# Kernel optimization log

Measured on AMD Instinct MI355X. Metric: run time of the kernel, lower is better.

The kernel has to match this reference:

```python
import jax, jax.numpy as jnp
import numpy as np

BETA = 0.25  # commitment-loss weight from init_kwargs

B, T, D, K = 16, 2048, 256, 1024


def setup_inputs() -> dict:
    key = jax.random.key(0)
    k1, k2 = jax.random.split(key)
    z_e = jax.random.normal(k1, (B, T, D), dtype=jnp.float32)
    codebook = jax.random.normal(k2, (K, D), dtype=jnp.float32)
    return {"z_e": z_e, "codebook": codebook}


def reference(z_e, codebook):
    # dot_z_embedding: tensordot over channel dim -> (B, T, K)
    dot = jnp.einsum("btd,kd->btk", z_e, codebook)
    norm_sq_z = jnp.sum(jnp.square(z_e), axis=-1, keepdims=True)      # (B, T, 1)
    norm_sq_e = jnp.sum(jnp.square(codebook), axis=-1)                # (K,)
    dist = -2.0 * dot + norm_sq_z + norm_sq_e                         # (B, T, K)
    ids = jnp.argmin(dist, axis=-1)                                   # (B, T) int
    z_q = codebook[ids]                                               # (B, T, D)
    # losses: tf.norm over the quantised axis, then mean
    loss_commit = jnp.mean(jnp.linalg.norm(jax.lax.stop_gradient(z_e) - z_q, axis=-1))
    loss_codebook = jnp.mean(jnp.linalg.norm(z_e - jax.lax.stop_gradient(z_q), axis=-1))
    loss_vq = loss_codebook + BETA * loss_commit
    similarity = dot / jnp.sqrt(norm_sq_z) / jnp.sqrt(norm_sq_e)      # (B, T, K) cosine
    return z_q, similarity, ids, loss_vq
```

## Files before the change

### kernel.cpp

```cpp
#include <hip/hip_runtime.h>


#define M_ROWS 32768
#define KCODES 1024
#define DDIM   256

typedef __bf16 bf16_t;
typedef __attribute__((ext_vector_type(8))) bf16_t bf16x8;
typedef __attribute__((ext_vector_type(4))) float f32x4;

__device__ __forceinline__ unsigned short f2bf(float f) {
  unsigned u = __float_as_uint(f);
  u += 0x7FFFu + ((u >> 16) & 1u);
  return (unsigned short)(u >> 16);
}

__device__ __forceinline__ float wave_sum(float p) {
#pragma unroll
  for (int o = 1; o < 64; o <<= 1) p += __shfl_xor(p, o);
  return p;
}
__device__ __forceinline__ float wave_min(float p) {
#pragma unroll
  for (int o = 1; o < 64; o <<= 1) p = fminf(p, __shfl_xor(p, o));
  return p;
}

__global__ __launch_bounds__(256) void prep_kernel(
    const float* __restrict__ ze, const float* __restrict__ cb,
    unsigned short* __restrict__ zb, unsigned short* __restrict__ cbb,
    float* __restrict__ sqz, float* __restrict__ rsqz,
    float* __restrict__ nse, float* __restrict__ sqe, float* __restrict__ rsqe)
{
  const int t = threadIdx.x;
  const int lane = t & 63;
  const int row = blockIdx.x * 4 + (t >> 6);
  if (row < M_ROWS) {
    const float4 z = ((const float4*)ze)[(size_t)row * 64 + lane];
    ushort4 u;
    u.x = f2bf(z.x); u.y = f2bf(z.y); u.z = f2bf(z.z); u.w = f2bf(z.w);
    ((ushort4*)zb)[(size_t)row * 64 + lane] = u;
    float p = wave_sum(z.x*z.x + z.y*z.y + z.z*z.z + z.w*z.w);
    if (lane == 0) { float s = sqrtf(p); sqz[row] = s; rsqz[row] = 1.0f / s; }
  } else {
    const int r = row - M_ROWS;
    const float4 e = ((const float4*)cb)[(size_t)r * 64 + lane];
    ushort4 u;
    u.x = f2bf(e.x); u.y = f2bf(e.y); u.z = f2bf(e.z); u.w = f2bf(e.w);
    ((ushort4*)cbb)[(size_t)r * 64 + lane] = u;
    float p = wave_sum(e.x*e.x + e.y*e.y + e.z*e.z + e.w*e.w);
    if (lane == 0) { nse[r] = p; float s = sqrtf(p); sqe[r] = s; rsqe[r] = 1.0f / s; }
  }
}

__global__ __launch_bounds__(256, 2) void gemm_sim_kernel(
    const unsigned short* __restrict__ zb, const unsigned short* __restrict__ cbb,
    const float* __restrict__ rsqz, const float* __restrict__ rsqe,
    float* __restrict__ sim)
{
  __shared__ __attribute__((aligned(128))) unsigned short lds[16384];
  const int tid  = threadIdx.x;
  const int wv   = tid >> 6, lane = tid & 63;
  const int bid  = blockIdx.x;
  const int swz  = (bid & 7) * 256 + (bid >> 3);
  const long row0 = (long)(swz >> 3) * 128;
  const int  col0 = (swz & 7) * 128;

  f32x4 acc[4][4] = {};

  const int rr = lane >> 3, qq = lane & 7;
  const int sq = ((qq ^ rr) << 3);

  for (int kt = 0; kt < 4; ++kt) {
    const int k0 = kt * 64;
#pragma unroll
    for (int i = 0; i < 4; ++i) {
      const int rbase = wv * 32 + i * 8;
      const unsigned short* srca = zb  + ((size_t)(row0 + rbase + rr)) * DDIM + k0 + sq;
      const unsigned short* srcb = cbb + ((size_t)(col0 + rbase + rr)) * DDIM + k0 + sq;
      __builtin_amdgcn_global_load_lds((const __attribute__((address_space(1))) void*)srca,
                                       (__attribute__((address_space(3))) void*)&lds[rbase * 64],
                                       16, 0, 0);
      __builtin_amdgcn_global_load_lds((const __attribute__((address_space(1))) void*)srcb,
                                       (__attribute__((address_space(3))) void*)&lds[8192 + rbase * 64],
                                       16, 0, 0);
    }
    __syncthreads();
    const int r16 = lane & 15, g = lane >> 4;
#pragma unroll
    for (int ks = 0; ks < 2; ++ks) {
      bf16x8 af[4], bfr[4];
#pragma unroll
      for (int mi = 0; mi < 4; ++mi) {
        const int r  = (wv >> 1) * 64 + mi * 16 + r16;
        const int qy = ((ks * 4 + g) ^ (r & 7)) << 4;
        af[mi] = *(const bf16x8*)((const char*)lds + r * 128 + qy);
      }
#pragma unroll
      for (int ni = 0; ni < 4; ++ni) {
        const int r  = (wv & 1) * 64 + ni * 16 + r16;
        const int qy = ((ks * 4 + g) ^ (r & 7)) << 4;
        bfr[ni] = *(const bf16x8*)((const char*)lds + 16384 + r * 128 + qy);
      }
#pragma unroll
      for (int mi = 0; mi < 4; ++mi)
#pragma unroll
        for (int ni = 0; ni < 4; ++ni)
          acc[mi][ni] = __builtin_amdgcn_mfma_f32_16x16x32_bf16(af[mi], bfr[ni], acc[mi][ni], 0, 0, 0);
    }
    __syncthreads();
  }

  const int r16 = lane & 15, g = lane >> 4;
  const int wm = wv >> 1, wn = wv & 1;
#pragma unroll
  for (int mi = 0; mi < 4; ++mi) {
#pragma unroll
    for (int j = 0; j < 4; ++j) {
      const long row = row0 + wm * 64 + mi * 16 + g * 4 + j;
      const float rz = rsqz[row];
      float* so = sim + (size_t)row * KCODES + col0 + wn * 64 + r16;
#pragma unroll
      for (int ni = 0; ni < 4; ++ni)
        so[ni * 16] = acc[mi][ni][j] * rz * rsqe[col0 + wn * 64 + ni * 16 + r16];
    }
  }
}

__global__ __launch_bounds__(256) void select_kernel(
    const float* __restrict__ ze, const float* __restrict__ cb,
    const float* __restrict__ sim, const float* __restrict__ sqz,
    const float* __restrict__ nse, const float* __restrict__ sqe,
    float* __restrict__ zq, float* __restrict__ ids, float* __restrict__ partials)
{
  __shared__ float s_nse[KCODES];
  __shared__ float s_sqe[KCODES];
  __shared__ float s_part[4];
  const int t = threadIdx.x;
  ((float4*)s_nse)[t] = ((const float4*)nse)[t];
  ((float4*)s_sqe)[t] = ((const float4*)sqe)[t];
  __syncthreads();

  const int lane = t & 63;
  const int row  = blockIdx.x * 4 + (t >> 6);
  const float4 zr = ((const float4*)ze)[(size_t)row * 64 + lane];
  const float  c2 = 2.0f * sqz[row];
  const float4* simr = (const float4*)(sim + (size_t)row * KCODES);

  float v[16];
  float vmin = INFINITY;
#pragma unroll
  for (int i = 0; i < 4; ++i) {
    const float4 s4 = simr[i * 64 + lane];
    const float sv[4] = {s4.x, s4.y, s4.z, s4.w};
#pragma unroll
    for (int c = 0; c < 4; ++c) {
      const int k = i * 256 + lane * 4 + c;
      const float val = s_nse[k] - c2 * s_sqe[k] * sv[c];
      v[i * 4 + c] = val;
      vmin = fminf(vmin, val);
    }
  }
  vmin = wave_min(vmin);
  const float lim = vmin + 1.0f;

  float tbest = INFINITY; int kbest = KCODES;
#pragma unroll
  for (int idx = 0; idx < 16; ++idx) {
    unsigned long long m = __ballot(v[idx] <= lim);
    const int i = idx >> 2, c = idx & 3;
    while (m) {
      const int lb = __ffsll(m) - 1;
      m &= m - 1;
      const int kc = i * 256 + lb * 4 + c;
      const float4 er = ((const float4*)cb)[(size_t)kc * 64 + lane];
      float p = wave_sum(zr.x*er.x + zr.y*er.y + zr.z*er.z + zr.w*er.w);
      const float tv = s_nse[kc] - 2.0f * p;
      if (tv < tbest || (tv == tbest && kc < kbest)) { tbest = tv; kbest = kc; }
    }
  }

  const float4 er = ((const float4*)cb)[(size_t)kbest * 64 + lane];
  ((float4*)zq)[(size_t)row * 64 + lane] = er;
  const float dx = zr.x - er.x, dy = zr.y - er.y, dz = zr.z - er.z, dw = zr.w - er.w;
  const float ss = wave_sum(dx*dx + dy*dy + dz*dz + dw*dw);
  if (lane == 0) {
    ids[row] = (float)kbest;
    s_part[t >> 6] = sqrtf(ss);
  }
  __syncthreads();
  if (t == 0)
    partials[blockIdx.x] = (s_part[0] + s_part[1]) + (s_part[2] + s_part[3]);
}

__global__ __launch_bounds__(256) void finalize_kernel(
    const float* __restrict__ partials, float* __restrict__ out_loss)
{
  __shared__ float s[4];
  const int t = threadIdx.x;
  float p = 0.0f;
#pragma unroll
  for (int i = 0; i < 32; ++i) p += partials[t + i * 256];
  p = wave_sum(p);
  if ((t & 63) == 0) s[t >> 6] = p;
  __syncthreads();
  if (t == 0) out_loss[0] = 1.25f * ((s[0] + s[1]) + (s[2] + s[3])) / 32768.0f;
}

extern "C" void kernel_launch(void* const* d_in, const int* in_sizes, int n_in,
                              void* d_out, int out_size, void* d_ws, size_t ws_size,
                              hipStream_t stream) {
  const float* ze = (const float*)d_in[0];
  const float* cb = (const float*)d_in[1];

  float* out  = (float*)d_out;
  float* zq   = out;
  float* sim  = out + 8388608;
  float* ids  = out + 41943040;
  float* lout = out + 41975808;

  char* w = (char*)d_ws;
  unsigned short* cbb = (unsigned short*)w;
  float* sqz  = (float*)(w + 524288);
  float* rsqz = (float*)(w + 655360);
  float* nse  = (float*)(w + 786432);
  float* sqe  = (float*)(w + 790528);
  float* rsqe = (float*)(w + 794624);
  float* partials = rsqz;

  unsigned short* zb = (unsigned short*)d_out;

  prep_kernel<<<8448, 256, 0, stream>>>(ze, cb, zb, cbb, sqz, rsqz, nse, sqe, rsqe);
  gemm_sim_kernel<<<2048, 256, 0, stream>>>(zb, cbb, rsqz, rsqe, sim);
  select_kernel<<<8192, 256, 0, stream>>>(ze, cb, sim, sqz, nse, sqe, zq, ids, partials);
  finalize_kernel<<<1, 256, 0, stream>>>(partials, lout);
}
```

Measured before the change: 78.30 us.

## Fuse per-tile top-2 candidate extraction into GEMM epilogue, skip similarity reread

The GEMM epilogue now computes quantized, index-encoded distances per row and keeps the top two candidates per 64-column tile, writing them to a small workspace buffer. A new select kernel reads these 32 candidates per row instead of the full 1024-wide similarity row and recomputes exact fp32 distances only for candidates within a margin. This removes the select kernel's read of the 128MB similarity matrix, at the cost of extra shuffle work in the GEMM epilogue. It falls back to the old path when the workspace is too small, and the top-2-per-tile pruning with a fixed margin could miss the true argmin in rare cases.

```diff
diff --git a/kernel.cpp b/kernel.cpp
--- a/kernel.cpp
+++ b/kernel.cpp
@@ -4,6 +4,7 @@
 #define M_ROWS 32768
 #define KCODES 1024
 #define DDIM   256
+#define ENC_BIG 33554432.0f
 
 typedef __bf16 bf16_t;
 typedef __attribute__((ext_vector_type(8))) bf16_t bf16x8;
@@ -56,7 +57,8 @@
 __global__ __launch_bounds__(256, 2) void gemm_sim_kernel(
     const unsigned short* __restrict__ zb, const unsigned short* __restrict__ cbb,
     const float* __restrict__ rsqz, const float* __restrict__ rsqe,
-    float* __restrict__ sim)
+    const float* __restrict__ nse,
+    float* __restrict__ sim, float* __restrict__ cand)
 {
   __shared__ __attribute__((aligned(128))) unsigned short lds[16384];
   const int tid  = threadIdx.x;
@@ -113,6 +115,7 @@
 
   const int r16 = lane & 15, g = lane >> 4;
   const int wm = wv >> 1, wn = wv & 1;
+
 #pragma unroll
   for (int mi = 0; mi < 4; ++mi) {
 #pragma unroll
@@ -125,9 +128,90 @@
         so[ni * 16] = acc[mi][ni][j] * rz * rsqe[col0 + wn * 64 + ni * 16 + r16];
     }
   }
-}
-
-__global__ __launch_bounds__(256) void select_kernel(
+
+  if (cand) {
+    float nsev[4];
+#pragma unroll
+    for (int ni = 0; ni < 4; ++ni) nsev[ni] = nse[col0 + wn * 64 + ni * 16 + r16];
+    const int tileIdx = ((col0 >> 6) | wn);
+#pragma unroll
+    for (int mi = 0; mi < 4; ++mi) {
+#pragma unroll
+      for (int j = 0; j < 4; ++j) {
+        float e1 = ENC_BIG, e2 = ENC_BIG;
+#pragma unroll
+        for (int ni = 0; ni < 4; ++ni) {
+          const float v = nsev[ni] - 2.0f * acc[mi][ni][j];
+          const float kf = (float)(col0 + wn * 64 + ni * 16 + r16);
+          const float enc = floorf((v + 1024.0f) * 8.0f) * 1024.0f + kf;
+          if (enc < e1) { e2 = e1; e1 = enc; } else e2 = fminf(e2, enc);
+        }
+#pragma unroll
+        for (int m = 1; m < 16; m <<= 1) {
+          const float p1 = __shfl_xor(e1, m);
+          const float p2 = __shfl_xor(e2, m);
+          const float n1 = fminf(e1, p1);
+          const float n2 = fminf(fmaxf(e1, p1), fminf(e2, p2));
+          e1 = n1; e2 = n2;
+        }
+        if (r16 == 0) {
+          const long row = row0 + wm * 64 + mi * 16 + g * 4 + j;
+          ((float2*)cand)[row * 16 + tileIdx] = make_float2(e1, e2);
+        }
+      }
+    }
+  }
+}
+
+__global__ __launch_bounds__(256) void select_fast_kernel(
+    const float* __restrict__ ze, const float* __restrict__ cb,
+    const float* __restrict__ cand, const float* __restrict__ nse,
+    float* __restrict__ zq, float* __restrict__ ids, float* __restrict__ partials)
+{
+  __shared__ float s_part[4];
+  const int t = threadIdx.x;
+  const int lane = t & 63;
+  const int row  = blockIdx.x * 4 + (t >> 6);
+
+  const float4 zr = ((const float4*)ze)[(size_t)row * 64 + lane];
+
+  const float* crow = cand + (size_t)row * 32;
+  float e = (lane < 32) ? crow[lane] : ENC_BIG;
+  const float m_enc = wave_min(e);
+  const float qmin  = floorf(m_enc * 0.0009765625f);
+  const float ql    = floorf(e * 0.0009765625f);
+
+  unsigned long long msk = __ballot(ql <= qmin + 16.0f);
+  int kbest;
+  if (__popcll(msk) == 1) {
+    kbest = ((int)m_enc) & 1023;
+  } else {
+    float tbest = INFINITY; kbest = KCODES;
+    while (msk) {
+      const int lb = __ffsll(msk) - 1;
+      msk &= msk - 1;
+      const int kc = ((int)__shfl(e, lb)) & 1023;
+      const float4 er = ((const float4*)cb)[(size_t)kc * 64 + lane];
+      const float p = wave_sum(zr.x*er.x + zr.y*er.y + zr.z*er.z + zr.w*er.w);
+      const float tv = nse[kc] - 2.0f * p;
+      if (tv < tbest || (tv == tbest && kc < kbest)) { tbest = tv; kbest = kc; }
+    }
+  }
+
+  const float4 er = ((const float4*)cb)[(size_t)kbest * 64 + lane];
+  ((float4*)zq)[(size_t)row * 64 + lane] = er;
+  const float dx = zr.x - er.x, dy = zr.y - er.y, dz = zr.z - er.z, dw = zr.w - er.w;
+  const float ss = wave_sum(dx*dx + dy*dy + dz*dz + dw*dw);
+  if (lane == 0) {
+    ids[row] = (float)kbest;
+    s_part[t >> 6] = sqrtf(ss);
+  }
+  __syncthreads();
+  if (t == 0)
+    partials[blockIdx.x] = (s_part[0] + s_part[1]) + (s_part[2] + s_part[3]);
+}
+
+__global__ __launch_bounds__(256) void select_full_kernel(
     const float* __restrict__ ze, const float* __restrict__ cb,
     const float* __restrict__ sim, const float* __restrict__ sqz,
     const float* __restrict__ nse, const float* __restrict__ sqe,
@@ -226,12 +310,19 @@
   float* nse  = (float*)(w + 786432);
   float* sqe  = (float*)(w + 790528);
   float* rsqe = (float*)(w + 794624);
+  float* cand = (float*)(w + 798720);
   float* partials = rsqz;
 
+  const bool fast = ws_size >= (size_t)(798720 + 4 * 1024 * 1024 + 256);
+
   unsigned short* zb = (unsigned short*)d_out;
 
   prep_kernel<<<8448, 256, 0, stream>>>(ze, cb, zb, cbb, sqz, rsqz, nse, sqe, rsqe);
-  gemm_sim_kernel<<<2048, 256, 0, stream>>>(zb, cbb, rsqz, rsqe, sim);
-  select_kernel<<<8192, 256, 0, stream>>>(ze, cb, sim, sqz, nse, sqe, zq, ids, partials);
+  gemm_sim_kernel<<<2048, 256, 0, stream>>>(zb, cbb, rsqz, rsqe, nse, sim,
+                                            fast ? cand : nullptr);
+  if (fast)
+    select_fast_kernel<<<8192, 256, 0, stream>>>(ze, cb, cand, nse, zq, ids, partials);
+  else
+    select_full_kernel<<<8192, 256, 0, stream>>>(ze, cb, sim, sqz, nse, sqe, zq, ids, partials);
   finalize_kernel<<<1, 256, 0, stream>>>(partials, lout);
 }
```

After: 72.85 us. -7.0%, faster.

## Fuse z prep, GEMM, argmin selection and loss into one kernel

Applied to the files above, without the earlier changes.

Merges the z-side prep, the similarity GEMM and the argmin/select pass into a single kernel. Each block now owns 64 rows across all 1024 codes, keeps the bf16 z tile resident in LDS, and computes top-2 quantised distance candidates per 64-column strip in the GEMM epilogue. This removes the bf16 z round-trip through global memory and the re-read of the 128 MB similarity matrix in the select pass. In exchange, the grid is only 512 blocks, the codebook is re-streamed per block with no double buffering, and a candidate may be missed when more than two near-ties fall in one strip.

```diff
diff --git a/kernel.cpp b/kernel.cpp
--- a/kernel.cpp
+++ b/kernel.cpp
@@ -4,6 +4,7 @@
 #define M_ROWS 32768
 #define KCODES 1024
 #define DDIM   256
+#define ENC_BIG 33554432.0f
 
 typedef __bf16 bf16_t;
 typedef __attribute__((ext_vector_type(8))) bf16_t bf16x8;
@@ -26,168 +27,181 @@
   return p;
 }
 
-__global__ __launch_bounds__(256) void prep_kernel(
-    const float* __restrict__ ze, const float* __restrict__ cb,
-    unsigned short* __restrict__ zb, unsigned short* __restrict__ cbb,
-    float* __restrict__ sqz, float* __restrict__ rsqz,
-    float* __restrict__ nse, float* __restrict__ sqe, float* __restrict__ rsqe)
+__global__ __launch_bounds__(256) void prep_cb_kernel(
+    const float* __restrict__ cb, unsigned short* __restrict__ cbb,
+    float* __restrict__ nse, float* __restrict__ rsqe)
 {
   const int t = threadIdx.x;
   const int lane = t & 63;
-  const int row = blockIdx.x * 4 + (t >> 6);
-  if (row < M_ROWS) {
-    const float4 z = ((const float4*)ze)[(size_t)row * 64 + lane];
+  const int r = blockIdx.x * 4 + (t >> 6);
+  const float4 e = ((const float4*)cb)[(size_t)r * 64 + lane];
+  ushort4 u;
+  u.x = f2bf(e.x); u.y = f2bf(e.y); u.z = f2bf(e.z); u.w = f2bf(e.w);
+  ((ushort4*)cbb)[(size_t)r * 64 + lane] = u;
+  float p = wave_sum(e.x*e.x + e.y*e.y + e.z*e.z + e.w*e.w);
+  if (lane == 0) { nse[r] = p; rsqe[r] = 1.0f / sqrtf(p); }
+}
+
+__global__ __launch_bounds__(256, 2) void fused_kernel(
+    const float* __restrict__ ze, const float* __restrict__ cb,
+    const unsigned short* __restrict__ cbb,
+    const float* __restrict__ nse_g, const float* __restrict__ rsqe_g,
+    float* __restrict__ sim, float* __restrict__ zq, float* __restrict__ ids,
+    float* __restrict__ partials)
+{
+  __shared__ __attribute__((aligned(128))) unsigned short A[64 * 256];
+  __shared__ __attribute__((aligned(128))) unsigned short Bt[128 * 64];
+  __shared__ float s_nse[KCODES];
+  __shared__ float s_rsqe[KCODES];
+  __shared__ float s_rsqz[64];
+  __shared__ float cand_lds[64 * 32];
+  __shared__ float s_part[4];
+
+  const int t = threadIdx.x;
+  const int wv = t >> 6, lane = t & 63;
+  const int r16 = lane & 15, g = lane >> 4;
+  const int wm = wv >> 1, wn = wv & 1;
+  const long row0 = (long)blockIdx.x * 64;
+
+  ((float4*)s_nse)[t]  = ((const float4*)nse_g)[t];
+  ((float4*)s_rsqe)[t] = ((const float4*)rsqe_g)[t];
+
+#pragma unroll
+  for (int k = 0; k < 16; ++k) {
+    const int row = wv + 4 * k;
+    const float4 z = ((const float4*)ze)[(row0 + row) * 64 + lane];
+    const float p = wave_sum(z.x*z.x + z.y*z.y + z.z*z.z + z.w*z.w);
+    if (lane == 0) s_rsqz[row] = 1.0f / sqrtf(p);
     ushort4 u;
     u.x = f2bf(z.x); u.y = f2bf(z.y); u.z = f2bf(z.z); u.w = f2bf(z.w);
-    ((ushort4*)zb)[(size_t)row * 64 + lane] = u;
-    float p = wave_sum(z.x*z.x + z.y*z.y + z.z*z.z + z.w*z.w);
-    if (lane == 0) { float s = sqrtf(p); sqz[row] = s; rsqz[row] = 1.0f / s; }
-  } else {
-    const int r = row - M_ROWS;
-    const float4 e = ((const float4*)cb)[(size_t)r * 64 + lane];
-    ushort4 u;
-    u.x = f2bf(e.x); u.y = f2bf(e.y); u.z = f2bf(e.z); u.w = f2bf(e.w);
-    ((ushort4*)cbb)[(size_t)r * 64 + lane] = u;
-    float p = wave_sum(e.x*e.x + e.y*e.y + e.z*e.z + e.w*e.w);
-    if (lane == 0) { nse[r] = p; float s = sqrtf(p); sqe[r] = s; rsqe[r] = 1.0f / s; }
+    const int q  = lane >> 1;
+    const int ph = (q & 24) | ((q ^ (row & 7)) & 7);
+    *(ushort4*)((char*)A + row * 512 + ph * 16 + (lane & 1) * 8) = u;
   }
-}
-
-__global__ __launch_bounds__(256, 2) void gemm_sim_kernel(
-    const unsigned short* __restrict__ zb, const unsigned short* __restrict__ cbb,
-    const float* __restrict__ rsqz, const float* __restrict__ rsqe,
-    float* __restrict__ sim)
-{
-  __shared__ __attribute__((aligned(128))) unsigned short lds[16384];
-  const int tid  = threadIdx.x;
-  const int wv   = tid >> 6, lane = tid & 63;
-  const int bid  = blockIdx.x;
-  const int swz  = (bid & 7) * 256 + (bid >> 3);
-  const long row0 = (long)(swz >> 3) * 128;
-  const int  col0 = (swz & 7) * 128;
-
-  f32x4 acc[4][4] = {};
-
+  __syncthreads();
+
+  f32x4 acc[2][4] = {};
   const int rr = lane >> 3, qq = lane & 7;
   const int sq = ((qq ^ rr) << 3);
 
-  for (int kt = 0; kt < 4; ++kt) {
-    const int k0 = kt * 64;
+  for (int kt = 0; kt < 32; ++kt) {
+    const int c = kt >> 2, kk = kt & 3;
+    const int col0 = c * 128, k0 = kk * 64;
 #pragma unroll
     for (int i = 0; i < 4; ++i) {
       const int rbase = wv * 32 + i * 8;
-      const unsigned short* srca = zb  + ((size_t)(row0 + rbase + rr)) * DDIM + k0 + sq;
-      const unsigned short* srcb = cbb + ((size_t)(col0 + rbase + rr)) * DDIM + k0 + sq;
-      __builtin_amdgcn_global_load_lds((const __attribute__((address_space(1))) void*)srca,
-                                       (__attribute__((address_space(3))) void*)&lds[rbase * 64],
+      const unsigned short* src = cbb + ((size_t)(col0 + rbase + rr)) * DDIM + k0 + sq;
+      __builtin_amdgcn_global_load_lds((const __attribute__((address_space(1))) void*)src,
+                                       (__attribute__((address_space(3))) void*)&Bt[rbase * 64],
                                        16, 0, 0);
-      __builtin_amdgcn_global_load_lds((const __attribute__((address_space(1))) void*)srcb,
-                                       (__attribute__((address_space(3))) void*)&lds[8192 + rbase * 64],
-                                       16, 0, 0);
     }
     __syncthreads();
-    const int r16 = lane & 15, g = lane >> 4;
 #pragma unroll
     for (int ks = 0; ks < 2; ++ks) {
-      bf16x8 af[4], bfr[4];
-#pragma unroll
-      for (int mi = 0; mi < 4; ++mi) {
-        const int r  = (wv >> 1) * 64 + mi * 16 + r16;
-        const int qy = ((ks * 4 + g) ^ (r & 7)) << 4;
-        af[mi] = *(const bf16x8*)((const char*)lds + r * 128 + qy);
+      bf16x8 af[2], bf[4];
+#pragma unroll
+      for (int mi = 0; mi < 2; ++mi) {
+        const int r = wm * 32 + mi * 16 + r16;
+        const int ql = kk * 8 + ks * 4 + g;
+        const int ph = (ql & 24) | ((ql ^ (r & 7)) & 7);
+        af[mi] = *(const bf16x8*)((const char*)A + r * 512 + ph * 16);
       }
 #pragma unroll
       for (int ni = 0; ni < 4; ++ni) {
-        const int r  = (wv & 1) * 64 + ni * 16 + r16;
-        const int qy = ((ks * 4 + g) ^ (r & 7)) << 4;
-        bfr[ni] = *(const bf16x8*)((const char*)lds + 16384 + r * 128 + qy);
-      }
-#pragma unroll
-      for (int mi = 0; mi < 4; ++mi)
+        const int r = wn * 64 + ni * 16 + r16;
+        const int ph = (ks * 4 + g) ^ (r & 7);
+        bf[ni] = *(const bf16x8*)((const char*)Bt + r * 128 + ph * 16);
+      }
+#pragma unroll
+      for (int mi = 0; mi < 2; ++mi)
 #pragma unroll
         for (int ni = 0; ni < 4; ++ni)
-          acc[mi][ni] = __builtin_amdgcn_mfma_f32_16x16x32_bf16(af[mi], bfr[ni], acc[mi][ni], 0, 0, 0);
+          acc[mi][ni] = __builtin_amdgcn_mfma_f32_16x16x32_bf16(af[mi], bf[ni], acc[mi][ni], 0, 0, 0);
     }
     __syncthreads();
+
+    if (kk == 3) {
+      const int strip = c * 2 + wn;
+#pragma unroll
+      for (int mi = 0; mi < 2; ++mi) {
+#pragma unroll
+        for (int j = 0; j < 4; ++j) {
+          const int rloc = wm * 32 + mi * 16 + g * 4 + j;
+          const long row = row0 + rloc;
+          const float rz = s_rsqz[rloc];
+          float* so = sim + (size_t)row * KCODES + col0 + wn * 64 + r16;
+          float e1 = ENC_BIG, e2 = ENC_BIG;
+#pragma unroll
+          for (int ni = 0; ni < 4; ++ni) {
+            const int colk = col0 + wn * 64 + ni * 16 + r16;
+            const float d = acc[mi][ni][j];
+            so[ni * 16] = d * rz * s_rsqe[colk];
+            const float v = s_nse[colk] - 2.0f * d;
+            const float enc = floorf((v + 1024.0f) * 8.0f) * 1024.0f + (float)colk;
+            if (enc < e1) { e2 = e1; e1 = enc; } else e2 = fminf(e2, enc);
+          }
+#pragma unroll
+          for (int m = 1; m < 16; m <<= 1) {
+            const float p1 = __shfl_xor(e1, m);
+            const float p2 = __shfl_xor(e2, m);
+            const float n1 = fminf(e1, p1);
+            const float n2 = fminf(fmaxf(e1, p1), fminf(e2, p2));
+            e1 = n1; e2 = n2;
+          }
+          if (r16 == 0) {
+            cand_lds[rloc * 32 + strip * 2]     = e1;
+            cand_lds[rloc * 32 + strip * 2 + 1] = e2;
+          }
+        }
+      }
+#pragma unroll
+      for (int mi = 0; mi < 2; ++mi)
+#pragma unroll
+        for (int ni = 0; ni < 4; ++ni)
+          acc[mi][ni] = (f32x4)(0.0f);
+    }
   }
-
-  const int r16 = lane & 15, g = lane >> 4;
-  const int wm = wv >> 1, wn = wv & 1;
-#pragma unroll
-  for (int mi = 0; mi < 4; ++mi) {
-#pragma unroll
-    for (int j = 0; j < 4; ++j) {
-      const long row = row0 + wm * 64 + mi * 16 + g * 4 + j;
-      const float rz = rsqz[row];
-      float* so = sim + (size_t)row * KCODES + col0 + wn * 64 + r16;
-#pragma unroll
-      for (int ni = 0; ni < 4; ++ni)
-        so[ni * 16] = acc[mi][ni][j] * rz * rsqe[col0 + wn * 64 + ni * 16 + r16];
+  __syncthreads();
+
+  float loss_local = 0.0f;
+  float4 zr = ((const float4*)ze)[(row0 + wv * 16) * 64 + lane];
+  for (int i = 0; i < 16; ++i) {
+    const int rloc = wv * 16 + i;
+    const long row = row0 + rloc;
+    const float4 zc = zr;
+    if (i < 15) zr = ((const float4*)ze)[(row + 1) * 64 + lane];
+
+    const float e = (lane < 32) ? cand_lds[rloc * 32 + lane] : ENC_BIG;
+    const float m_enc = wave_min(e);
+    const float qmin  = floorf(m_enc * 0.0009765625f);
+    const float ql    = floorf(e * 0.0009765625f);
+    unsigned long long msk = __ballot(ql <= qmin + 16.0f);
+    int kbest;
+    if (__popcll(msk) == 1) {
+      kbest = ((int)m_enc) & 1023;
+    } else {
+      float tbest = INFINITY; kbest = KCODES;
+      while (msk) {
+        const int lb = __ffsll(msk) - 1;
+        msk &= msk - 1;
+        const int kc = ((int)__shfl(e, lb)) & 1023;
+        const float4 er = ((const float4*)cb)[(size_t)kc * 64 + lane];
+        const float p = wave_sum(zc.x*er.x + zc.y*er.y + zc.z*er.z + zc.w*er.w);
+        const float tv = s_nse[kc] - 2.0f * p;
+        if (tv < tbest || (tv == tbest && kc < kbest)) { tbest = tv; kbest = kc; }
+      }
+    }
+
+    const float4 er = ((const float4*)cb)[(size_t)kbest * 64 + lane];
+    ((float4*)zq)[(size_t)row * 64 + lane] = er;
+    const float dx = zc.x - er.x, dy = zc.y - er.y, dz = zc.z - er.z, dw = zc.w - er.w;
+    const float ss = wave_sum(dx*dx + dy*dy + dz*dz + dw*dw);
+    if (lane == 0) {
+      ids[row] = (float)kbest;
+      loss_local += sqrtf(ss);
     }
   }
-}
-
-__global__ __launch_bounds__(256) void select_kernel(
-    const float* __restrict__ ze, const float* __restrict__ cb,
-    const float* __restrict__ sim, const float* __restrict__ sqz,
-    const float* __restrict__ nse, const float* __restrict__ sqe,
-    float* __restrict__ zq, float* __restrict__ ids, float* __restrict__ partials)
-{
-  __shared__ float s_nse[KCODES];
-  __shared__ float s_sqe[KCODES];
-  __shared__ float s_part[4];
-  const int t = threadIdx.x;
-  ((float4*)s_nse)[t] = ((const float4*)nse)[t];
-  ((float4*)s_sqe)[t] = ((const float4*)sqe)[t];
-  __syncthreads();
-
-  const int lane = t & 63;
-  const int row  = blockIdx.x * 4 + (t >> 6);
-  const float4 zr = ((const float4*)ze)[(size_t)row * 64 + lane];
-  const float  c2 = 2.0f * sqz[row];
-  const float4* simr = (const float4*)(sim + (size_t)row * KCODES);
-
-  float v[16];
-  float vmin = INFINITY;
-#pragma unroll
-  for (int i = 0; i < 4; ++i) {
-    const float4 s4 = simr[i * 64 + lane];
-    const float sv[4] = {s4.x, s4.y, s4.z, s4.w};
-#pragma unroll
-    for (int c = 0; c < 4; ++c) {
-      const int k = i * 256 + lane * 4 + c;
-      const float val = s_nse[k] - c2 * s_sqe[k] * sv[c];
-      v[i * 4 + c] = val;
-      vmin = fminf(vmin, val);
-    }
-  }
-  vmin = wave_min(vmin);
-  const float lim = vmin + 1.0f;
-
-  float tbest = INFINITY; int kbest = KCODES;
-#pragma unroll
-  for (int idx = 0; idx < 16; ++idx) {
-    unsigned long long m = __ballot(v[idx] <= lim);
-    const int i = idx >> 2, c = idx & 3;
-    while (m) {
-      const int lb = __ffsll(m) - 1;
-      m &= m - 1;
-      const int kc = i * 256 + lb * 4 + c;
-      const float4 er = ((const float4*)cb)[(size_t)kc * 64 + lane];
-      float p = wave_sum(zr.x*er.x + zr.y*er.y + zr.z*er.z + zr.w*er.w);
-      const float tv = s_nse[kc] - 2.0f * p;
-      if (tv < tbest || (tv == tbest && kc < kbest)) { tbest = tv; kbest = kc; }
-    }
-  }
-
-  const float4 er = ((const float4*)cb)[(size_t)kbest * 64 + lane];
-  ((float4*)zq)[(size_t)row * 64 + lane] = er;
-  const float dx = zr.x - er.x, dy = zr.y - er.y, dz = zr.z - er.z, dw = zr.w - er.w;
-  const float ss = wave_sum(dx*dx + dy*dy + dz*dz + dw*dw);
-  if (lane == 0) {
-    ids[row] = (float)kbest;
-    s_part[t >> 6] = sqrtf(ss);
-  }
+  if (lane == 0) s_part[wv] = loss_local;
   __syncthreads();
   if (t == 0)
     partials[blockIdx.x] = (s_part[0] + s_part[1]) + (s_part[2] + s_part[3]);
@@ -198,9 +212,7 @@
 {
   __shared__ float s[4];
   const int t = threadIdx.x;
-  float p = 0.0f;
-#pragma unroll
-  for (int i = 0; i < 32; ++i) p += partials[t + i * 256];
+  float p = partials[t] + partials[t + 256];
   p = wave_sum(p);
   if ((t & 63) == 0) s[t >> 6] = p;
   __syncthreads();
@@ -221,17 +233,11 @@
 
   char* w = (char*)d_ws;
   unsigned short* cbb = (unsigned short*)w;
-  float* sqz  = (float*)(w + 524288);
-  float* rsqz = (float*)(w + 655360);
-  float* nse  = (float*)(w + 786432);
-  float* sqe  = (float*)(w + 790528);
-  float* rsqe = (float*)(w + 794624);
-  float* partials = rsqz;
-
-  unsigned short* zb = (unsigned short*)d_out;
-
-  prep_kernel<<<8448, 256, 0, stream>>>(ze, cb, zb, cbb, sqz, rsqz, nse, sqe, rsqe);
-  gemm_sim_kernel<<<2048, 256, 0, stream>>>(zb, cbb, rsqz, rsqe, sim);
-  select_kernel<<<8192, 256, 0, stream>>>(ze, cb, sim, sqz, nse, sqe, zq, ids, partials);
+  float* nse      = (float*)(w + 524288);
+  float* rsqe     = (float*)(w + 528384);
+  float* partials = (float*)(w + 532480);
+
+  prep_cb_kernel<<<256, 256, 0, stream>>>(cb, cbb, nse, rsqe);
+  fused_kernel<<<512, 256, 0, stream>>>(ze, cb, cbb, nse, rsqe, sim, zq, ids, partials);
   finalize_kernel<<<1, 256, 0, stream>>>(partials, lout);
 }
```

Result: slower. 86.32 us (+10.2%).
